# Kernel tuning notes

Hardware: AMD Instinct MI355X
Metric: run time of the kernel (lower is better)

Reference implementation:

```python
import jax, jax.numpy as jnp
import numpy as np

C = 0.01          # Poincare ball curvature 1/100
SQRT_C = 0.1
EPS = 1e-15
BALL_EPS = 4e-3   # geoopt float32 projx boundary epsilon


def _norm(x):
    return jnp.linalg.norm(x, axis=-1, keepdims=True)


def expmap0(u):
    n = jnp.maximum(_norm(u), EPS)
    return jnp.tanh(SQRT_C * n) * u / (SQRT_C * n)


def logmap0(x):
    n = jnp.maximum(_norm(x), EPS)
    t = jnp.clip(SQRT_C * n, -1.0 + 1e-7, 1.0 - 1e-7)
    return jnp.arctanh(t) * x / (SQRT_C * n)


def projx(x):
    maxnorm = (1.0 - BALL_EPS) / SQRT_C
    n = jnp.maximum(_norm(x), EPS)
    return jnp.where(n > maxnorm, x / n * maxnorm, x)


def mobius_matvec(M, x):
    xn = jnp.maximum(_norm(x), EPS)
    mx = x @ M.T
    mxn = jnp.maximum(_norm(mx), EPS)
    t = jnp.clip(SQRT_C * xn, -1.0 + 1e-7, 1.0 - 1e-7)
    res = jnp.tanh(mxn / xn * jnp.arctanh(t)) * mx / (mxn * SQRT_C)
    return jnp.where(jnp.all(mx == 0, axis=-1, keepdims=True), 0.0, res)


def mobius_add(x, y):
    x2 = jnp.sum(x * x, -1, keepdims=True)
    y2 = jnp.sum(y * y, -1, keepdims=True)
    xy = jnp.sum(x * y, -1, keepdims=True)
    num = (1 + 2 * C * xy + C * y2) * x + (1 - C * x2) * y
    den = 1 + 2 * C * xy + C * C * x2 * y2
    return num / jnp.maximum(den, EPS)


def hyp_linear(x, W, b):
    # eval mode: weight dropout is a no-op
    res = projx(mobius_matvec(W, x))
    hb = projx(expmap0(b.reshape(1, -1)))
    return projx(mobius_add(res, hb))


def setup_inputs() -> dict:
    key = jax.random.key(0)
    ks = jax.random.split(key, 10)
    B, S, N, H, HEADS, E = 2, 4, 10000, 64, 4, 160000
    G = B * S
    OC = H // HEADS
    # edges guaranteed to have no self-loops (module removes then re-adds them)
    src = jax.random.randint(ks[0], (G, E), 0, N)
    off = jax.random.randint(ks[1], (G, E), 1, N)
    dst = (src + off) % N
    edge_index = jnp.stack([src, dst], axis=1).astype(jnp.int32)  # [G,2,E]

    def glorot(k, shape, fan):
        a = np.sqrt(6.0 / fan)
        return jax.random.uniform(k, shape, minval=-a, maxval=a, dtype=jnp.float32)

    emb = jax.random.normal(ks[2], (N, H), dtype=jnp.float32)
    att_i = glorot(ks[3], (1, HEADS, OC), HEADS * OC + 1)
    att_j = glorot(ks[4], (1, HEADS, OC), HEADS * OC + 1)
    w1 = glorot(ks[5], (H, OC), H + OC)   # HypLinear(in=16, out=64): weight [out,in]
    b1 = jnp.zeros((H,), jnp.float32)
    w2 = glorot(ks[6], (H, H), H + H)
    b2 = jnp.zeros((H,), jnp.float32)
    history_graphs = jnp.zeros((B, S, N), jnp.float32)  # only shape is used
    return {"history_graphs": history_graphs, "edge_index": edge_index,
            "emb": emb, "att_i": att_i, "att_j": att_j,
            "w1": w1, "b1": b1, "w2": w2, "b2": b2}


def reference(history_graphs, edge_index, emb, att_i, att_j, w1, b1, w2, b2):
    B, S, N = history_graphs.shape
    G = edge_index.shape[0]
    H = emb.shape[1]
    heads = att_i.shape[1]
    oc = H // heads

    # node ids are arange(N) for every (b,s) -> identical features per graph
    x0 = projx(expmap0(emb))   # initHyperX, [N,H]
    xt = logmap0(x0)           # tangent features used by attention, [N,H]

    # add self loops (inputs contain none)
    loops = jnp.broadcast_to(jnp.arange(N, dtype=edge_index.dtype)[None, None, :], (G, 2, N))
    ei = jnp.concatenate([edge_index, loops], axis=-1)  # [G,2,E+N]

    def agg(e):
        src, dst = e[0], e[1]                       # targets (i), sources (j)
        x_i = xt[src].reshape(-1, heads, oc)        # [E2,h,oc]
        x_j = xt[dst].reshape(-1, heads, oc)
        alpha = jnp.sum(x_i * att_i, -1) + jnp.sum(x_j * att_j, -1)  # [E2,h]
        alpha = jax.nn.leaky_relu(alpha, 0.2)
        m = jax.ops.segment_max(alpha, src, num_segments=N)
        a = jnp.exp(alpha - m[src])
        s = jax.ops.segment_sum(a, src, num_segments=N)
        a = a / (s[src] + 1e-16)                    # edge softmax; dropout eval no-op
        sup = jax.ops.segment_sum(x_j * a[..., None], src, num_segments=N)  # [N,h,oc]
        sup = sup.mean(axis=1)                      # concat=False -> head mean, [N,oc]
        return projx(expmap0(sup))

    h = jax.vmap(agg)(ei)                           # [G,N,oc]
    node_emb = h.reshape(B, S, N, oc)[:, -1]        # last timestep, [B,N,oc]

    z = hyp_linear(node_emb, w1, b1)                # 16 -> 64
    z = projx(expmap0(jax.nn.silu(logmap0(z))))     # HypAct(SiLU)
    z = projx(expmap0(logmap0(z)))                  # HypDropout (eval: log/exp round trip)
    z = hyp_linear(z, w2, b2)                       # 64 -> 64
    return z
```

## Files before the change

### kernel.cpp

```cpp
#include <hip/hip_runtime.h>
#include <hip/hip_bf16.h>

#define N_NODES 10000
#define NE 160000
#define CAP 96
#define SQRT_C 0.1f
#define CC 0.01f
#define EPS 1e-15f
#define MAXNORM ((1.0f - 4e-3f) / SQRT_C)

__device__ __forceinline__ float ldf(const void* p, int i, int isbf) {
    return isbf ? __bfloat162float(((const __hip_bfloat16*)p)[i])
                : ((const float*)p)[i];
}

__device__ __forceinline__ float wsum(float v) {
#pragma unroll
    for (int off = 32; off > 0; off >>= 1) v += __shfl_xor(v, off, 64);
    return v;
}
__device__ __forceinline__ float wmax(float v) {
#pragma unroll
    for (int off = 32; off > 0; off >>= 1) v = fmaxf(v, __shfl_xor(v, off, 64));
    return v;
}

__global__ __launch_bounds__(256) void init_sniff(int* __restrict__ cnt,
                                                  int* __restrict__ ovf_cnt,
                                                  const unsigned* __restrict__ embw,
                                                  int* __restrict__ flag) {
    int t = blockIdx.x * 256 + threadIdx.x;
    if (t < 2 * N_NODES) cnt[t] = 0;
    if (t == 0) *ovf_cnt = 0;
    if (blockIdx.x == 0 && threadIdx.x < 64) {
        unsigned w = embw[threadIdx.x];
        unsigned e = (w >> 7) & 0xFFu;
        unsigned long long m = __ballot(e >= 116u && e <= 133u);
        if (threadIdx.x == 0) *flag = (__popcll(m) >= 32) ? 1 : 0;
    }
}

#define EDGE_PREAMBLE(T)                                                  \
    int slot = ((T) >= NE) ? 1 : 0;                                       \
    int e = (T) - slot * NE;                                              \
    int g = slot ? 7 : 3;

__global__ __launch_bounds__(256) void pre_scatter(const void* __restrict__ emb,
                                                   const void* __restrict__ att_i,
                                                   const void* __restrict__ att_j,
                                                   const void* __restrict__ w1g,
                                                   const void* __restrict__ b1g,
                                                   const void* __restrict__ w2g,
                                                   const void* __restrict__ b2g,
                                                   const int* __restrict__ flag,
                                                   const int* __restrict__ ei,
                                                   float* __restrict__ xt,
                                                   float* __restrict__ ai,
                                                   float* __restrict__ aj,
                                                   int* __restrict__ cnt,
                                                   unsigned short* __restrict__ bucket,
                                                   int* __restrict__ ovf_cnt,
                                                   unsigned* __restrict__ ovf,
                                                   float* __restrict__ wf1t,
                                                   float* __restrict__ wf2t,
                                                   float* __restrict__ hb1f,
                                                   float* __restrict__ hb2f,
                                                   float* __restrict__ hbn2) {
    if (blockIdx.x < 2500) {
        int isbf = *flag;
        int t = blockIdx.x * 256 + threadIdx.x;
        int node = t >> 6;
        int lane = t & 63;
        float u = ldf(emb, node * 64 + lane, isbf);
        float n = fmaxf(sqrtf(wsum(u * u)), EPS);
        float th = tanhf(SQRT_C * n);
        float x0 = th / (SQRT_C * n) * u;
        float x0n = th / SQRT_C;
        if (x0n > MAXNORM) { x0 *= MAXNORM / x0n; x0n = MAXNORM; }
        float tc = fminf(SQRT_C * x0n, 1.0f - 1e-7f);
        float xv = atanhf(tc) / (SQRT_C * x0n) * x0;
        xt[node * 64 + lane] = xv;
        float pi = xv * ldf(att_i, lane, isbf);
        float pj = xv * ldf(att_j, lane, isbf);
#pragma unroll
        for (int off = 8; off > 0; off >>= 1) {
            pi += __shfl_xor(pi, off, 64);
            pj += __shfl_xor(pj, off, 64);
        }
        if ((lane & 15) == 0) {
            ai[node * 4 + (lane >> 4)] = pi;
            aj[node * 4 + (lane >> 4)] = pj;
        }
    } else if (blockIdx.x < 3750) {
        int t = (blockIdx.x - 2500) * 256 + threadIdx.x;
        EDGE_PREAMBLE(t);
        int src = ei[g * 2 * NE + e];
        int dst = ei[g * 2 * NE + NE + e];
        int i = slot * N_NODES + src;
        int pos = atomicAdd(&cnt[i], 1);
        if (pos < CAP) bucket[i * CAP + pos] = (unsigned short)dst;
        else {
            int oi = atomicAdd(ovf_cnt, 1);
            ovf[oi] = ((unsigned)slot << 28) | ((unsigned)src << 14) | (unsigned)dst;
        }
    } else {
        int isbf = *flag;
        int tid = threadIdx.x;
        for (int i = tid; i < 1024; i += 256) {
            int o = i >> 4, c = i & 15;
            wf1t[c * 64 + o] = ldf(w1g, i, isbf);
        }
        for (int i = tid; i < 4096; i += 256) {
            int o = i >> 6, c = i & 63;
            wf2t[c * 64 + o] = ldf(w2g, i, isbf);
        }
        int w = tid >> 6, lane = tid & 63;
        if (w < 2) {
            const void* bg = w ? b2g : b1g;
            float b = ldf(bg, lane, isbf);
            float n = fmaxf(sqrtf(wsum(b * b)), EPS);
            float th = tanhf(SQRT_C * n);
            float hv = th / (SQRT_C * n) * b;
            float hn = th / SQRT_C;
            if (hn > MAXNORM) { hv *= MAXNORM / hn; hn = MAXNORM; }
            (w ? hb2f : hb1f)[lane] = hv;
            if (lane == 0) hbn2[w] = hn * hn;
        }
    }
}

__global__ __launch_bounds__(256) void node_agg(const int* __restrict__ cnt,
                                                const unsigned short* __restrict__ bucket,
                                                const int* __restrict__ ovf_cnt,
                                                const unsigned* __restrict__ ovf,
                                                const float* __restrict__ ai,
                                                const float* __restrict__ aj,
                                                const float* __restrict__ xt,
                                                float* __restrict__ sup_t) {
    __shared__ float wlds[4][64 * 4];
    __shared__ int dlds[4][64];
    int w = threadIdx.x >> 6, lane = threadIdx.x & 63;
    int idx = blockIdx.x * 4 + w;
    int slot = (idx >= N_NODES) ? 1 : 0;
    int n = idx - slot * N_NODES;
    int deg = cnt[idx];
    int start = idx * CAP;

    float4 ai4 = *(const float4*)&ai[n * 4];
    float4 aj4n = *(const float4*)&aj[n * 4];
    float ain[4] = {ai4.x, ai4.y, ai4.z, ai4.w};
    float ajn[4] = {aj4n.x, aj4n.y, aj4n.z, aj4n.w};
    int hh = lane >> 4;
    float acc;

    if (deg <= 63) {
        bool act = (lane <= deg);
        int d = (lane < deg) ? (int)bucket[start + lane] : n;
        float4 a4 = act ? *(const float4*)&aj[d * 4] : make_float4(0.f, 0.f, 0.f, 0.f);
        float ajv[4] = {a4.x, a4.y, a4.z, a4.w};
        float al[4], mh[4], eh[4];
#pragma unroll
        for (int h = 0; h < 4; ++h) {
            float a = ain[h] + ajv[h];
            a = (a < 0.0f) ? 0.2f * a : a;
            al[h] = act ? a : -1e30f;
            mh[h] = al[h];
        }
#pragma unroll
        for (int h = 0; h < 4; ++h) mh[h] = wmax(mh[h]);
#pragma unroll
        for (int h = 0; h < 4; ++h) eh[h] = act ? expf(al[h] - mh[h]) : 0.0f;
        float sh[4];
#pragma unroll
        for (int h = 0; h < 4; ++h) sh[h] = wsum(eh[h]);
#pragma unroll
        for (int h = 0; h < 4; ++h)
            wlds[w][lane * 4 + h] = eh[h] * (0.25f / (sh[h] + 1e-16f));
        dlds[w][lane] = d;
        int m = deg + 1;
        float a0 = 0.f, a1 = 0.f, a2 = 0.f, a3 = 0.f;
        int e = 0;
        for (; e + 4 <= m; e += 4) {
            int d0 = dlds[w][e], d1 = dlds[w][e + 1];
            int d2 = dlds[w][e + 2], d3 = dlds[w][e + 3];
            float w0 = wlds[w][(e + 0) * 4 + hh], w1 = wlds[w][(e + 1) * 4 + hh];
            float w2 = wlds[w][(e + 2) * 4 + hh], w3 = wlds[w][(e + 3) * 4 + hh];
            a0 = fmaf(w0, xt[d0 * 64 + lane], a0);
            a1 = fmaf(w1, xt[d1 * 64 + lane], a1);
            a2 = fmaf(w2, xt[d2 * 64 + lane], a2);
            a3 = fmaf(w3, xt[d3 * 64 + lane], a3);
        }
        for (; e < m; ++e)
            a0 = fmaf(wlds[w][e * 4 + hh], xt[dlds[w][e] * 64 + lane], a0);
        acc = (a0 + a1) + (a2 + a3);
    } else {
        int bdeg = (deg < CAP) ? deg : CAP;
        int tov = (deg > CAP) ? *ovf_cnt : 0;
        float mh[4];
#pragma unroll
        for (int h = 0; h < 4; ++h) {
            float a = ain[h] + ajn[h];
            mh[h] = (a < 0.0f) ? 0.2f * a : a;
        }
        for (int e = lane; e < bdeg; e += 64) {
            int d = bucket[start + e];
#pragma unroll
            for (int h = 0; h < 4; ++h) {
                float a = ain[h] + aj[d * 4 + h];
                a = (a < 0.0f) ? 0.2f * a : a;
                mh[h] = fmaxf(mh[h], a);
            }
        }
        for (int k = lane; k < tov; k += 64) {
            unsigned pe = ovf[k];
            if ((int)(pe >> 28) == slot && (int)((pe >> 14) & 0x3FFFu) == n) {
                int d = pe & 0x3FFFu;
#pragma unroll
                for (int h = 0; h < 4; ++h) {
                    float a = ain[h] + aj[d * 4 + h];
                    a = (a < 0.0f) ? 0.2f * a : a;
                    mh[h] = fmaxf(mh[h], a);
                }
            }
        }
#pragma unroll
        for (int h = 0; h < 4; ++h) mh[h] = wmax(mh[h]);
        float sh[4] = {0.f, 0.f, 0.f, 0.f};
        if (lane == 0) {
#pragma unroll
            for (int h = 0; h < 4; ++h) {
                float a = ain[h] + ajn[h];
                a = (a < 0.0f) ? 0.2f * a : a;
                sh[h] = expf(a - mh[h]);
            }
        }
        for (int e = lane; e < bdeg; e += 64) {
            int d = bucket[start + e];
#pragma unroll
            for (int h = 0; h < 4; ++h) {
                float a = ain[h] + aj[d * 4 + h];
                a = (a < 0.0f) ? 0.2f * a : a;
                sh[h] += expf(a - mh[h]);
            }
        }
        for (int k = lane; k < tov; k += 64) {
            unsigned pe = ovf[k];
            if ((int)(pe >> 28) == slot && (int)((pe >> 14) & 0x3FFFu) == n) {
                int d = pe & 0x3FFFu;
#pragma unroll
                for (int h = 0; h < 4; ++h) {
                    float a = ain[h] + aj[d * 4 + h];
                    a = (a < 0.0f) ? 0.2f * a : a;
                    sh[h] += expf(a - mh[h]);
                }
            }
        }
#pragma unroll
        for (int h = 0; h < 4; ++h) sh[h] = wsum(sh[h]);
        float scale[4];
#pragma unroll
        for (int h = 0; h < 4; ++h) scale[h] = 0.25f / (sh[h] + 1e-16f);
        float aih = ain[hh], mhh = mh[hh], sch = scale[hh];
        float aself = aih + ajn[hh];
        aself = (aself < 0.0f) ? 0.2f * aself : aself;
        acc = expf(aself - mhh) * sch * xt[n * 64 + lane];
        for (int e = 0; e < bdeg; ++e) {
            int d = bucket[start + e];
            float a = aih + aj[d * 4 + hh];
            a = (a < 0.0f) ? 0.2f * a : a;
            acc = fmaf(expf(a - mhh) * sch, xt[d * 64 + lane], acc);
        }
        for (int k = 0; k < tov; ++k) {
            unsigned pe = ovf[k];
            if ((int)(pe >> 28) == slot && (int)((pe >> 14) & 0x3FFFu) == n) {
                int d = pe & 0x3FFFu;
                float a = aih + aj[d * 4 + hh];
                a = (a < 0.0f) ? 0.2f * a : a;
                acc = fmaf(expf(a - mhh) * sch, xt[d * 64 + lane], acc);
            }
        }
    }
    acc += __shfl_xor(acc, 16, 64);
    acc += __shfl_xor(acc, 32, 64);
    if (lane < 16) sup_t[lane * 20000 + idx] = acc;
}

__global__ __launch_bounds__(256) void final_stage(const float* __restrict__ sup_t,
                                                   const float* __restrict__ wf1t,
                                                   const float* __restrict__ wf2t,
                                                   const float* __restrict__ hb1f,
                                                   const float* __restrict__ hb2f,
                                                   const float* __restrict__ hbn2,
                                                   const int* __restrict__ flag,
                                                   void* __restrict__ outv) {
    __shared__ float Z[65 * 64];
    __shared__ float pA[2][4][64];
    __shared__ float pB[2][4][64];
    int w = threadIdx.x >> 6, lane = threadIdx.x & 63;
    int base = blockIdx.x * 64;
    int nd = base + lane;
    bool valid = (nd < 2 * N_NODES);
    int isbf = *flag;
    float y2a = hbn2[0], y2b = hbn2[1];
    int ob = w * 16;

    float v[16];
#pragma unroll
    for (int c = 0; c < 16; ++c) v[c] = valid ? sup_t[c * 20000 + nd] : 0.0f;
    float n2 = 0.f;
#pragma unroll
    for (int c = 0; c < 16; ++c) n2 = fmaf(v[c], v[c], n2);
    float n = fmaxf(sqrtf(n2), EPS);
    float th0 = tanhf(SQRT_C * n);
    float s0 = th0 / (SQRT_C * n);
    float x0n = th0 / SQRT_C;
    if (x0n > MAXNORM) { s0 *= MAXNORM / x0n; x0n = MAXNORM; }
#pragma unroll
    for (int c = 0; c < 16; ++c) v[c] *= s0;

    float a1[16];
#pragma unroll
    for (int oj = 0; oj < 16; ++oj) a1[oj] = 0.f;
#pragma unroll
    for (int c = 0; c < 16; ++c) {
        float vc = v[c];
#pragma unroll
        for (int oj = 0; oj < 16; ++oj)
            a1[oj] = fmaf(wf1t[c * 64 + ob + oj], vc, a1[oj]);
    }
    float pn = 0.f, ph = 0.f;
#pragma unroll
    for (int oj = 0; oj < 16; ++oj) {
        pn = fmaf(a1[oj], a1[oj], pn);
        ph = fmaf(a1[oj], hb1f[ob + oj], ph);
    }
    pA[0][w][lane] = pn; pA[1][w][lane] = ph;
    __syncthreads();
    float mxn2 = pA[0][0][lane] + pA[0][1][lane] + pA[0][2][lane] + pA[0][3][lane];
    float mxhb = pA[1][0][lane] + pA[1][1][lane] + pA[1][2][lane] + pA[1][3][lane];

    float z2n;
    {
        float xn = fmaxf(x0n, EPS);
        float mxn = fmaxf(sqrtf(mxn2), EPS);
        float t = fminf(SQRT_C * xn, 1.0f - 1e-7f);
        float th = tanhf(mxn / xn * atanhf(t));
        float rs = th / (mxn * SQRT_C);
        float rn = th / SQRT_C;
        if (mxn2 == 0.0f) { rs = 0.f; rn = 0.f; }
        if (rn > MAXNORM) { rs *= MAXNORM / rn; rn = MAXNORM; }
        float xy = rs * mxhb;
        float x2 = rn * rn;
        float A = 1.0f + 2.0f * CC * xy + CC * y2a;
        float B = 1.0f - CC * x2;
        float rden = 1.0f / fmaxf(1.0f + 2.0f * CC * xy + CC * CC * x2 * y2a, EPS);
        float pz = 0.f;
#pragma unroll
        for (int oj = 0; oj < 16; ++oj) {
            float z = (A * rs * a1[oj] + B * hb1f[ob + oj]) * rden;
            a1[oj] = z;
            pz = fmaf(z, z, pz);
        }
        pB[0][w][lane] = pz;
        __syncthreads();
        float zn2 = pB[0][0][lane] + pB[0][1][lane] + pB[0][2][lane] + pB[0][3][lane];
        float zn = fmaxf(sqrtf(zn2), EPS);
        float sc = (zn > MAXNORM) ? MAXNORM / zn : 1.0f;
        float z1n = fminf(zn, MAXNORM);
        float lg = atanhf(fminf(SQRT_C * z1n, 1.0f - 1e-7f)) / (SQRT_C * z1n) * sc;
        float pu = 0.f;
#pragma unroll
        for (int oj = 0; oj < 16; ++oj) {
            float u = lg * a1[oj];
            u = u / (1.0f + expf(-u));
            a1[oj] = u;
            pu = fmaf(u, u, pu);
        }
        pA[0][w][lane] = pu;
        __syncthreads();
        float un2 = pA[0][0][lane] + pA[0][1][lane] + pA[0][2][lane] + pA[0][3][lane];
        float un = fmaxf(sqrtf(un2), EPS);
        float th2 = tanhf(SQRT_C * un);
        float s2 = th2 / (SQRT_C * un);
        z2n = th2 / SQRT_C;
        if (z2n > MAXNORM) { s2 *= MAXNORM / z2n; z2n = MAXNORM; }
#pragma unroll
        for (int oj = 0; oj < 16; ++oj) Z[(ob + oj) * 64 + lane] = a1[oj] * s2;
    }
    __syncthreads();

    float a2[16];
#pragma unroll
    for (int oj = 0; oj < 16; ++oj) a2[oj] = 0.f;
#pragma unroll 4
    for (int c = 0; c < 64; ++c) {
        float zc = Z[c * 64 + lane];
#pragma unroll
        for (int oj = 0; oj < 16; ++oj)
            a2[oj] = fmaf(wf2t[c * 64 + ob + oj], zc, a2[oj]);
    }
    float pn2 = 0.f, ph2 = 0.f;
#pragma unroll
    for (int oj = 0; oj < 16; ++oj) {
        pn2 = fmaf(a2[oj], a2[oj], pn2);
        ph2 = fmaf(a2[oj], hb2f[ob + oj], ph2);
    }
    pB[0][w][lane] = pn2; pB[1][w][lane] = ph2;
    __syncthreads();
    float mxn2b = pB[0][0][lane] + pB[0][1][lane] + pB[0][2][lane] + pB[0][3][lane];
    float mxhb2 = pB[1][0][lane] + pB[1][1][lane] + pB[1][2][lane] + pB[1][3][lane];
    {
        float xn = fmaxf(z2n, EPS);
        float mxn = fmaxf(sqrtf(mxn2b), EPS);
        float t = fminf(SQRT_C * xn, 1.0f - 1e-7f);
        float th = tanhf(mxn / xn * atanhf(t));
        float rs = th / (mxn * SQRT_C);
        float rn = th / SQRT_C;
        if (mxn2b == 0.0f) { rs = 0.f; rn = 0.f; }
        if (rn > MAXNORM) { rs *= MAXNORM / rn; rn = MAXNORM; }
        float xy = rs * mxhb2;
        float x2 = rn * rn;
        float A = 1.0f + 2.0f * CC * xy + CC * y2b;
        float B = 1.0f - CC * x2;
        float rden = 1.0f / fmaxf(1.0f + 2.0f * CC * xy + CC * CC * x2 * y2b, EPS);
        float pz = 0.f;
#pragma unroll
        for (int oj = 0; oj < 16; ++oj) {
            float z = (A * rs * a2[oj] + B * hb2f[ob + oj]) * rden;
            a2[oj] = z;
            pz = fmaf(z, z, pz);
        }
        pA[0][w][lane] = pz;
        __syncthreads();
        float zn2 = pA[0][0][lane] + pA[0][1][lane] + pA[0][2][lane] + pA[0][3][lane];
        float zn = fmaxf(sqrtf(zn2), EPS);
        float s4 = (zn > MAXNORM) ? MAXNORM / zn : 1.0f;
#pragma unroll
        for (int oj = 0; oj < 16; ++oj) Z[(ob + oj) * 65 + lane] = a2[oj] * s4;
    }
    __syncthreads();

#pragma unroll 1
    for (int k = 0; k < 16; ++k) {
        int nl = w * 16 + k;
        int ng = base + nl;
        if (ng >= 2 * N_NODES) break;
        float val = Z[lane * 65 + nl];
        if (isbf) ((__hip_bfloat16*)outv)[ng * 64 + lane] = __float2bfloat16(val);
        else      ((float*)outv)[ng * 64 + lane] = val;
    }
}

extern "C" void kernel_launch(void* const* d_in, const int* in_sizes, int n_in,
                              void* d_out, int out_size, void* d_ws, size_t ws_size,
                              hipStream_t stream) {
    const int* ei = (const int*)d_in[1];
    const void* emb   = d_in[2];
    const void* att_i = d_in[3];
    const void* att_j = d_in[4];
    const void* w1 = d_in[5];
    const void* b1 = d_in[6];
    const void* w2 = d_in[7];
    const void* b2 = d_in[8];

    float* ws = (float*)d_ws;
    float* xt    = ws;
    float* ai    = ws + 640000;
    float* aj    = ws + 680000;
    float* sup_t = ws + 720000;
    int* cnt   = (int*)(ws + 1040000);
    unsigned short* bucket = (unsigned short*)(ws + 1060000);
    unsigned* ovf = (unsigned*)(ws + 2020000);
    int* ovf_cnt  = (int*)(ws + 2340000);
    int* flag     = (int*)(ws + 2340001);
    float* wf1t = ws + 2340032;
    float* wf2t = ws + 2341056;
    float* hb1f = ws + 2345152;
    float* hb2f = ws + 2345216;
    float* hbn2 = ws + 2345280;

    hipLaunchKernelGGL(init_sniff, dim3(79), dim3(256), 0, stream,
                       cnt, ovf_cnt, (const unsigned*)emb, flag);
    hipLaunchKernelGGL(pre_scatter, dim3(3751), dim3(256), 0, stream,
                       emb, att_i, att_j, w1, b1, w2, b2, flag, ei,
                       xt, ai, aj, cnt, bucket, ovf_cnt, ovf,
                       wf1t, wf2t, hb1f, hb2f, hbn2);
    hipLaunchKernelGGL(node_agg, dim3(5000), dim3(256), 0, stream,
                       cnt, bucket, ovf_cnt, ovf, ai, aj, xt, sup_t);
    hipLaunchKernelGGL(final_stage, dim3(313), dim3(256), 0, stream,
                       sup_t, wf1t, wf2t, hb1f, hb2f, hbn2, flag, d_out);
}
```

Before: 155.4 us.

## Fuse four kernel launches into one persistent kernel with grid barriers

Replaces the four separate launches (init, pre-scatter, node aggregation, final stage) with a single persistent kernel of 768 blocks that loops over the original block indices. Stages are separated by custom global atomic barriers that use open and done sentinel values. The goal is to remove the launch gaps and tail effects between small kernels. In exchange it relies on all 768 blocks being co-resident, adds spin-wait barrier latency, and grid-strides the work, which may lower per-stage parallelism.

Result: slower. 606.4 us (+290.3%).

```diff
diff --git a/kernel.cpp b/kernel.cpp
--- a/kernel.cpp
+++ b/kernel.cpp
@@ -4,6 +4,7 @@
 #define N_NODES 10000
 #define NE 160000
 #define CAP 96
+#define GRID 768
 #define SQRT_C 0.1f
 #define CC 0.01f
 #define EPS 1e-15f
@@ -25,19 +26,30 @@
     return v;
 }
 
-__global__ __launch_bounds__(256) void init_sniff(int* __restrict__ cnt,
-                                                  int* __restrict__ ovf_cnt,
-                                                  const unsigned* __restrict__ embw,
-                                                  int* __restrict__ flag) {
-    int t = blockIdx.x * 256 + threadIdx.x;
-    if (t < 2 * N_NODES) cnt[t] = 0;
-    if (t == 0) *ovf_cnt = 0;
-    if (blockIdx.x == 0 && threadIdx.x < 64) {
-        unsigned w = embw[threadIdx.x];
-        unsigned e = (w >> 7) & 0xFFu;
-        unsigned long long m = __ballot(e >= 116u && e <= 133u);
-        if (threadIdx.x == 0) *flag = (__popcll(m) >= 32) ? 1 : 0;
+#define M_OPEN(i) (0x13570000 + 2 * (i))
+#define M_DONE(i) (0x13570001 + 2 * (i))
+__device__ __forceinline__ void gbar(int* cnt, int* gen, int i, int G) {
+    __syncthreads();
+    if (threadIdx.x == 0) {
+        __threadfence();
+        for (long k = 0; k < (1L << 26); ++k) {
+            if (__hip_atomic_load(gen, __ATOMIC_ACQUIRE, __HIP_MEMORY_SCOPE_AGENT)
+                == M_OPEN(i)) break;
+            __builtin_amdgcn_s_sleep(8);
+        }
+        if (atomicAdd(cnt, 1) == G - 1) {
+            __hip_atomic_store(gen, M_DONE(i), __ATOMIC_RELEASE,
+                               __HIP_MEMORY_SCOPE_AGENT);
+        } else {
+            for (long k = 0; k < (1L << 26); ++k) {
+                if (__hip_atomic_load(gen, __ATOMIC_ACQUIRE, __HIP_MEMORY_SCOPE_AGENT)
+                    == M_DONE(i)) break;
+                __builtin_amdgcn_s_sleep(8);
+            }
+        }
     }
+    __syncthreads();
+    __threadfence();
 }
 
 #define EDGE_PREAMBLE(T)                                                  \
@@ -45,176 +57,185 @@
     int e = (T) - slot * NE;                                              \
     int g = slot ? 7 : 3;
 
-__global__ __launch_bounds__(256) void pre_scatter(const void* __restrict__ emb,
-                                                   const void* __restrict__ att_i,
-                                                   const void* __restrict__ att_j,
-                                                   const void* __restrict__ w1g,
-                                                   const void* __restrict__ b1g,
-                                                   const void* __restrict__ w2g,
-                                                   const void* __restrict__ b2g,
-                                                   const int* __restrict__ flag,
-                                                   const int* __restrict__ ei,
-                                                   float* __restrict__ xt,
-                                                   float* __restrict__ ai,
-                                                   float* __restrict__ aj,
-                                                   int* __restrict__ cnt,
-                                                   unsigned short* __restrict__ bucket,
-                                                   int* __restrict__ ovf_cnt,
-                                                   unsigned* __restrict__ ovf,
-                                                   float* __restrict__ wf1t,
-                                                   float* __restrict__ wf2t,
-                                                   float* __restrict__ hb1f,
-                                                   float* __restrict__ hb2f,
-                                                   float* __restrict__ hbn2) {
-    if (blockIdx.x < 2500) {
-        int isbf = *flag;
-        int t = blockIdx.x * 256 + threadIdx.x;
-        int node = t >> 6;
-        int lane = t & 63;
-        float u = ldf(emb, node * 64 + lane, isbf);
-        float n = fmaxf(sqrtf(wsum(u * u)), EPS);
-        float th = tanhf(SQRT_C * n);
-        float x0 = th / (SQRT_C * n) * u;
-        float x0n = th / SQRT_C;
-        if (x0n > MAXNORM) { x0 *= MAXNORM / x0n; x0n = MAXNORM; }
-        float tc = fminf(SQRT_C * x0n, 1.0f - 1e-7f);
-        float xv = atanhf(tc) / (SQRT_C * x0n) * x0;
-        xt[node * 64 + lane] = xv;
-        float pi = xv * ldf(att_i, lane, isbf);
-        float pj = xv * ldf(att_j, lane, isbf);
-#pragma unroll
-        for (int off = 8; off > 0; off >>= 1) {
-            pi += __shfl_xor(pi, off, 64);
-            pj += __shfl_xor(pj, off, 64);
-        }
-        if ((lane & 15) == 0) {
-            ai[node * 4 + (lane >> 4)] = pi;
-            aj[node * 4 + (lane >> 4)] = pj;
-        }
-    } else if (blockIdx.x < 3750) {
-        int t = (blockIdx.x - 2500) * 256 + threadIdx.x;
-        EDGE_PREAMBLE(t);
-        int src = ei[g * 2 * NE + e];
-        int dst = ei[g * 2 * NE + NE + e];
-        int i = slot * N_NODES + src;
-        int pos = atomicAdd(&cnt[i], 1);
-        if (pos < CAP) bucket[i * CAP + pos] = (unsigned short)dst;
-        else {
-            int oi = atomicAdd(ovf_cnt, 1);
-            ovf[oi] = ((unsigned)slot << 28) | ((unsigned)src << 14) | (unsigned)dst;
-        }
-    } else {
-        int isbf = *flag;
-        int tid = threadIdx.x;
-        for (int i = tid; i < 1024; i += 256) {
-            int o = i >> 4, c = i & 15;
-            wf1t[c * 64 + o] = ldf(w1g, i, isbf);
-        }
-        for (int i = tid; i < 4096; i += 256) {
-            int o = i >> 6, c = i & 63;
-            wf2t[c * 64 + o] = ldf(w2g, i, isbf);
-        }
-        int w = tid >> 6, lane = tid & 63;
-        if (w < 2) {
-            const void* bg = w ? b2g : b1g;
-            float b = ldf(bg, lane, isbf);
-            float n = fmaxf(sqrtf(wsum(b * b)), EPS);
+__global__ __launch_bounds__(256, 4) void fused(const int* __restrict__ ei,
+                                                const void* __restrict__ emb,
+                                                const void* __restrict__ att_i,
+                                                const void* __restrict__ att_j,
+                                                const void* __restrict__ w1g,
+                                                const void* __restrict__ b1g,
+                                                const void* __restrict__ w2g,
+                                                const void* __restrict__ b2g,
+                                                float* __restrict__ xt,
+                                                float* __restrict__ ai,
+                                                float* __restrict__ aj,
+                                                float* __restrict__ sup_t,
+                                                int* __restrict__ cnt,
+                                                unsigned short* __restrict__ bucket,
+                                                int* __restrict__ ovf_cnt,
+                                                unsigned* __restrict__ ovf,
+                                                int* __restrict__ flag,
+                                                float* __restrict__ wf1t,
+                                                float* __restrict__ wf2t,
+                                                float* __restrict__ hb1f,
+                                                float* __restrict__ hb2f,
+                                                float* __restrict__ hbn2,
+                                                int* __restrict__ bar,
+                                                void* __restrict__ outv) {
+    __shared__ float smem[5184];
+    const int G = gridDim.x;
+    int tid = threadIdx.x;
+    int w = tid >> 6, lane = tid & 63;
+
+    for (int t = blockIdx.x * 256 + tid; t < 2 * N_NODES; t += G * 256) cnt[t] = 0;
+    if (blockIdx.x == 0 && tid < 64) {
+        unsigned wv = ((const unsigned*)emb)[tid];
+        unsigned ex = (wv >> 7) & 0xFFu;
+        unsigned long long m = __ballot(ex >= 116u && ex <= 133u);
+        if (tid == 0) {
+            *flag = (__popcll(m) >= 32) ? 1 : 0;
+            *ovf_cnt = 0;
+            bar[0] = 0; bar[32] = 0; bar[64] = 0;
+            __threadfence();
+            __hip_atomic_store(&bar[16], M_OPEN(0), __ATOMIC_RELEASE,
+                               __HIP_MEMORY_SCOPE_AGENT);
+            __hip_atomic_store(&bar[48], M_OPEN(1), __ATOMIC_RELEASE,
+                               __HIP_MEMORY_SCOPE_AGENT);
+            __hip_atomic_store(&bar[80], M_OPEN(2), __ATOMIC_RELEASE,
+                               __HIP_MEMORY_SCOPE_AGENT);
+        }
+    }
+    gbar(&bar[0], &bar[16], 0, G);
+    int isbf = *flag;
+
+    for (int lb = blockIdx.x; lb < 3751; lb += G) {
+        if (lb < 2500) {
+            int t = lb * 256 + tid;
+            int node = t >> 6;
+            float u = ldf(emb, node * 64 + lane, isbf);
+            float n = fmaxf(sqrtf(wsum(u * u)), EPS);
             float th = tanhf(SQRT_C * n);
-            float hv = th / (SQRT_C * n) * b;
-            float hn = th / SQRT_C;
-            if (hn > MAXNORM) { hv *= MAXNORM / hn; hn = MAXNORM; }
-            (w ? hb2f : hb1f)[lane] = hv;
-            if (lane == 0) hbn2[w] = hn * hn;
+            float x0 = th / (SQRT_C * n) * u;
+            float x0n = th / SQRT_C;
+            if (x0n > MAXNORM) { x0 *= MAXNORM / x0n; x0n = MAXNORM; }
+            float tc = fminf(SQRT_C * x0n, 1.0f - 1e-7f);
+            float xv = atanhf(tc) / (SQRT_C * x0n) * x0;
+            xt[node * 64 + lane] = xv;
+            float pi = xv * ldf(att_i, lane, isbf);
+            float pj = xv * ldf(att_j, lane, isbf);
+#pragma unroll
+            for (int off = 8; off > 0; off >>= 1) {
+                pi += __shfl_xor(pi, off, 64);
+                pj += __shfl_xor(pj, off, 64);
+            }
+            if ((lane & 15) == 0) {
+                ai[node * 4 + (lane >> 4)] = pi;
+                aj[node * 4 + (lane >> 4)] = pj;
+            }
+        } else if (lb < 3750) {
+            int t = (lb - 2500) * 256 + tid;
+            EDGE_PREAMBLE(t);
+            int src = ei[g * 2 * NE + e];
+            int dst = ei[g * 2 * NE + NE + e];
+            int i = slot * N_NODES + src;
+            int pos = atomicAdd(&cnt[i], 1);
+            if (pos < CAP) bucket[i * CAP + pos] = (unsigned short)dst;
+            else {
+                int oi = atomicAdd(ovf_cnt, 1);
+                ovf[oi] = ((unsigned)slot << 28) | ((unsigned)src << 14) | (unsigned)dst;
+            }
+        } else {
+            for (int i = tid; i < 1024; i += 256) {
+                int o = i >> 4, c = i & 15;
+                wf1t[c * 64 + o] = ldf(w1g, i, isbf);
+            }
+            for (int i = tid; i < 4096; i += 256) {
+                int o = i >> 6, c = i & 63;
+                wf2t[c * 64 + o] = ldf(w2g, i, isbf);
+            }
+            if (w < 2) {
+                const void* bg = w ? b2g : b1g;
+                float b = ldf(bg, lane, isbf);
+                float n = fmaxf(sqrtf(wsum(b * b)), EPS);
+                float th = tanhf(SQRT_C * n);
+                float hv = th / (SQRT_C * n) * b;
+                float hn = th / SQRT_C;
+                if (hn > MAXNORM) { hv *= MAXNORM / hn; hn = MAXNORM; }
+                (w ? hb2f : hb1f)[lane] = hv;
+                if (lane == 0) hbn2[w] = hn * hn;
+            }
         }
     }
-}
-
-__global__ __launch_bounds__(256) void node_agg(const int* __restrict__ cnt,
-                                                const unsigned short* __restrict__ bucket,
-                                                const int* __restrict__ ovf_cnt,
-                                                const unsigned* __restrict__ ovf,
-                                                const float* __restrict__ ai,
-                                                const float* __restrict__ aj,
-                                                const float* __restrict__ xt,
-                                                float* __restrict__ sup_t) {
-    __shared__ float wlds[4][64 * 4];
-    __shared__ int dlds[4][64];
-    int w = threadIdx.x >> 6, lane = threadIdx.x & 63;
-    int idx = blockIdx.x * 4 + w;
-    int slot = (idx >= N_NODES) ? 1 : 0;
-    int n = idx - slot * N_NODES;
-    int deg = cnt[idx];
-    int start = idx * CAP;
-
-    float4 ai4 = *(const float4*)&ai[n * 4];
-    float4 aj4n = *(const float4*)&aj[n * 4];
-    float ain[4] = {ai4.x, ai4.y, ai4.z, ai4.w};
-    float ajn[4] = {aj4n.x, aj4n.y, aj4n.z, aj4n.w};
-    int hh = lane >> 4;
-    float acc;
-
-    if (deg <= 63) {
-        bool act = (lane <= deg);
-        int d = (lane < deg) ? (int)bucket[start + lane] : n;
-        float4 a4 = act ? *(const float4*)&aj[d * 4] : make_float4(0.f, 0.f, 0.f, 0.f);
-        float ajv[4] = {a4.x, a4.y, a4.z, a4.w};
-        float al[4], mh[4], eh[4];
-#pragma unroll
-        for (int h = 0; h < 4; ++h) {
-            float a = ain[h] + ajv[h];
-            a = (a < 0.0f) ? 0.2f * a : a;
-            al[h] = act ? a : -1e30f;
-            mh[h] = al[h];
-        }
-#pragma unroll
-        for (int h = 0; h < 4; ++h) mh[h] = wmax(mh[h]);
-#pragma unroll
-        for (int h = 0; h < 4; ++h) eh[h] = act ? expf(al[h] - mh[h]) : 0.0f;
-        float sh[4];
-#pragma unroll
-        for (int h = 0; h < 4; ++h) sh[h] = wsum(eh[h]);
-#pragma unroll
-        for (int h = 0; h < 4; ++h)
-            wlds[w][lane * 4 + h] = eh[h] * (0.25f / (sh[h] + 1e-16f));
-        dlds[w][lane] = d;
-        int m = deg + 1;
-        float a0 = 0.f, a1 = 0.f, a2 = 0.f, a3 = 0.f;
-        int e = 0;
-        for (; e + 4 <= m; e += 4) {
-            int d0 = dlds[w][e], d1 = dlds[w][e + 1];
-            int d2 = dlds[w][e + 2], d3 = dlds[w][e + 3];
-            float w0 = wlds[w][(e + 0) * 4 + hh], w1 = wlds[w][(e + 1) * 4 + hh];
-            float w2 = wlds[w][(e + 2) * 4 + hh], w3 = wlds[w][(e + 3) * 4 + hh];
-            a0 = fmaf(w0, xt[d0 * 64 + lane], a0);
-            a1 = fmaf(w1, xt[d1 * 64 + lane], a1);
-            a2 = fmaf(w2, xt[d2 * 64 + lane], a2);
-            a3 = fmaf(w3, xt[d3 * 64 + lane], a3);
-        }
-        for (; e < m; ++e)
-            a0 = fmaf(wlds[w][e * 4 + hh], xt[dlds[w][e] * 64 + lane], a0);
-        acc = (a0 + a1) + (a2 + a3);
-    } else {
-        int bdeg = (deg < CAP) ? deg : CAP;
-        int tov = (deg > CAP) ? *ovf_cnt : 0;
-        float mh[4];
-#pragma unroll
-        for (int h = 0; h < 4; ++h) {
-            float a = ain[h] + ajn[h];
-            mh[h] = (a < 0.0f) ? 0.2f * a : a;
-        }
-        for (int e = lane; e < bdeg; e += 64) {
-            int d = bucket[start + e];
+    gbar(&bar[32], &bar[48], 1, G);
+
+    float* wlds = smem;
+    int* dlds = (int*)&smem[1024];
+    for (int lb = blockIdx.x; lb < 5000; lb += G) {
+        int idx = lb * 4 + w;
+        int slot = (idx >= N_NODES) ? 1 : 0;
+        int n = idx - slot * N_NODES;
+        int deg = cnt[idx];
+        int start = idx * CAP;
+
+        float4 ai4 = *(const float4*)&ai[n * 4];
+        float4 aj4n = *(const float4*)&aj[n * 4];
+        float ain[4] = {ai4.x, ai4.y, ai4.z, ai4.w};
+        float ajn[4] = {aj4n.x, aj4n.y, aj4n.z, aj4n.w};
+        int hh = lane >> 4;
+        float acc;
+
+        if (deg <= 63) {
+            bool act = (lane <= deg);
+            int d = (lane < deg) ? (int)bucket[start + lane] : n;
+            float4 a4 = act ? *(const float4*)&aj[d * 4] : make_float4(0.f, 0.f, 0.f, 0.f);
+            float ajv[4] = {a4.x, a4.y, a4.z, a4.w};
+            float al[4], mh[4], eh[4];
 #pragma unroll
             for (int h = 0; h < 4; ++h) {
-                float a = ain[h] + aj[d * 4 + h];
+                float a = ain[h] + ajv[h];
                 a = (a < 0.0f) ? 0.2f * a : a;
-                mh[h] = fmaxf(mh[h], a);
-            }
-        }
-        for (int k = lane; k < tov; k += 64) {
-            unsigned pe = ovf[k];
-            if ((int)(pe >> 28) == slot && (int)((pe >> 14) & 0x3FFFu) == n) {
-                int d = pe & 0x3FFFu;
+                al[h] = act ? a : -1e30f;
+                mh[h] = al[h];
+            }
+#pragma unroll
+            for (int h = 0; h < 4; ++h) mh[h] = wmax(mh[h]);
+#pragma unroll
+            for (int h = 0; h < 4; ++h) eh[h] = act ? expf(al[h] - mh[h]) : 0.0f;
+            float sh[4];
+#pragma unroll
+            for (int h = 0; h < 4; ++h) sh[h] = wsum(eh[h]);
+#pragma unroll
+            for (int h = 0; h < 4; ++h)
+                wlds[w * 256 + lane * 4 + h] = eh[h] * (0.25f / (sh[h] + 1e-16f));
+            dlds[w * 64 + lane] = d;
+            int m = deg + 1;
+            float a0 = 0.f, a1 = 0.f, a2 = 0.f, a3 = 0.f;
+            int e = 0;
+            for (; e + 4 <= m; e += 4) {
+                int d0 = dlds[w * 64 + e], d1 = dlds[w * 64 + e + 1];
+                int d2 = dlds[w * 64 + e + 2], d3 = dlds[w * 64 + e + 3];
+                float w0 = wlds[w * 256 + (e + 0) * 4 + hh];
+                float w1 = wlds[w * 256 + (e + 1) * 4 + hh];
+                float w2 = wlds[w * 256 + (e + 2) * 4 + hh];
+                float w3 = wlds[w * 256 + (e + 3) * 4 + hh];
+                a0 = fmaf(w0, xt[d0 * 64 + lane], a0);
+                a1 = fmaf(w1, xt[d1 * 64 + lane], a1);
+                a2 = fmaf(w2, xt[d2 * 64 + lane], a2);
+                a3 = fmaf(w3, xt[d3 * 64 + lane], a3);
+            }
+            for (; e < m; ++e)
+                a0 = fmaf(wlds[w * 256 + e * 4 + hh], xt[dlds[w * 64 + e] * 64 + lane], a0);
+            acc = (a0 + a1) + (a2 + a3);
+        } else {
+            int bdeg = (deg < CAP) ? deg : CAP;
+            int tov = (deg > CAP) ? *ovf_cnt : 0;
+            float mh[4];
+#pragma unroll
+            for (int h = 0; h < 4; ++h) {
+                float a = ain[h] + ajn[h];
+                mh[h] = (a < 0.0f) ? 0.2f * a : a;
+            }
+            for (int e = lane; e < bdeg; e += 64) {
+                int d = bucket[start + e];
 #pragma unroll
                 for (int h = 0; h < 4; ++h) {
                     float a = ain[h] + aj[d * 4 + h];
@@ -222,31 +243,31 @@
                     mh[h] = fmaxf(mh[h], a);
                 }
             }
-        }
-#pragma unroll
-        for (int h = 0; h < 4; ++h) mh[h] = wmax(mh[h]);
-        float sh[4] = {0.f, 0.f, 0.f, 0.f};
-        if (lane == 0) {
-#pragma unroll
-            for (int h = 0; h < 4; ++h) {
-                float a = ain[h] + ajn[h];
-                a = (a < 0.0f) ? 0.2f * a : a;
-                sh[h] = expf(a - mh[h]);
-            }
-        }
-        for (int e = lane; e < bdeg; e += 64) {
-            int d = bucket[start + e];
-#pragma unroll
-            for (int h = 0; h < 4; ++h) {
-                float a = ain[h] + aj[d * 4 + h];
-                a = (a < 0.0f) ? 0.2f * a : a;
-                sh[h] += expf(a - mh[h]);
-            }
-        }
-        for (int k = lane; k < tov; k += 64) {
-            unsigned pe = ovf[k];
-            if ((int)(pe >> 28) == slot && (int)((pe >> 14) & 0x3FFFu) == n) {
-                int d = pe & 0x3FFFu;
+            for (int k = lane; k < tov; k += 64) {
+                unsigned pe = ovf[k];
+                if ((int)(pe >> 28) == slot && (int)((pe >> 14) & 0x3FFFu) == n) {
+                    int d = pe & 0x3FFFu;
+#pragma unroll
+                    for (int h = 0; h < 4; ++h) {
+                        float a = ain[h] + aj[d * 4 + h];
+                        a = (a < 0.0f) ? 0.2f * a : a;
+                        mh[h] = fmaxf(mh[h], a);
+                    }
+                }
+            }
+#pragma unroll
+            for (int h = 0; h < 4; ++h) mh[h] = wmax(mh[h]);
+            float sh[4] = {0.f, 0.f, 0.f, 0.f};
+            if (lane == 0) {
+#pragma unroll
+                for (int h = 0; h < 4; ++h) {
+                    float a = ain[h] + ajn[h];
+                    a = (a < 0.0f) ? 0.2f * a : a;
+                    sh[h] = expf(a - mh[h]);
+                }
+            }
+            for (int e = lane; e < bdeg; e += 64) {
+                int d = bucket[start + e];
 #pragma unroll
                 for (int h = 0; h < 4; ++h) {
                     float a = ain[h] + aj[d * 4 + h];
@@ -254,200 +275,209 @@
                     sh[h] += expf(a - mh[h]);
                 }
             }
-        }
-#pragma unroll
-        for (int h = 0; h < 4; ++h) sh[h] = wsum(sh[h]);
-        float scale[4];
-#pragma unroll
-        for (int h = 0; h < 4; ++h) scale[h] = 0.25f / (sh[h] + 1e-16f);
-        float aih = ain[hh], mhh = mh[hh], sch = scale[hh];
-        float aself = aih + ajn[hh];
-        aself = (aself < 0.0f) ? 0.2f * aself : aself;
-        acc = expf(aself - mhh) * sch * xt[n * 64 + lane];
-        for (int e = 0; e < bdeg; ++e) {
-            int d = bucket[start + e];
-            float a = aih + aj[d * 4 + hh];
-            a = (a < 0.0f) ? 0.2f * a : a;
-            acc = fmaf(expf(a - mhh) * sch, xt[d * 64 + lane], acc);
-        }
-        for (int k = 0; k < tov; ++k) {
-            unsigned pe = ovf[k];
-            if ((int)(pe >> 28) == slot && (int)((pe >> 14) & 0x3FFFu) == n) {
-                int d = pe & 0x3FFFu;
+            for (int k = lane; k < tov; k += 64) {
+                unsigned pe = ovf[k];
+                if ((int)(pe >> 28) == slot && (int)((pe >> 14) & 0x3FFFu) == n) {
+                    int d = pe & 0x3FFFu;
+#pragma unroll
+                    for (int h = 0; h < 4; ++h) {
+                        float a = ain[h] + aj[d * 4 + h];
+                        a = (a < 0.0f) ? 0.2f * a : a;
+                        sh[h] += expf(a - mh[h]);
+                    }
+                }
+            }
+#pragma unroll
+            for (int h = 0; h < 4; ++h) sh[h] = wsum(sh[h]);
+            float scale[4];
+#pragma unroll
+            for (int h = 0; h < 4; ++h) scale[h] = 0.25f / (sh[h] + 1e-16f);
+            float aih = ain[hh], mhh = mh[hh], sch = scale[hh];
+            float aself = aih + ajn[hh];
+            aself = (aself < 0.0f) ? 0.2f * aself : aself;
+            acc = expf(aself - mhh) * sch * xt[n * 64 + lane];
+            for (int e = 0; e < bdeg; ++e) {
+                int d = bucket[start + e];
                 float a = aih + aj[d * 4 + hh];
                 a = (a < 0.0f) ? 0.2f * a : a;
                 acc = fmaf(expf(a - mhh) * sch, xt[d * 64 + lane], acc);
             }
-        }
+            for (int k = 0; k < tov; ++k) {
+                unsigned pe = ovf[k];
+                if ((int)(pe >> 28) == slot && (int)((pe >> 14) & 0x3FFFu) == n) {
+                    int d = pe & 0x3FFFu;
+                    float a = aih + aj[d * 4 + hh];
+                    a = (a < 0.0f) ? 0.2f * a : a;
+                    acc = fmaf(expf(a - mhh) * sch, xt[d * 64 + lane], acc);
+                }
+            }
+        }
+        acc += __shfl_xor(acc, 16, 64);
+        acc += __shfl_xor(acc, 32, 64);
+        if (lane < 16) sup_t[lane * 20000 + idx] = acc;
     }
-    acc += __shfl_xor(acc, 16, 64);
-    acc += __shfl_xor(acc, 32, 64);
-    if (lane < 16) sup_t[lane * 20000 + idx] = acc;
-}
-
-__global__ __launch_bounds__(256) void final_stage(const float* __restrict__ sup_t,
-                                                   const float* __restrict__ wf1t,
-                                                   const float* __restrict__ wf2t,
-                                                   const float* __restrict__ hb1f,
-                                                   const float* __restrict__ hb2f,
-                                                   const float* __restrict__ hbn2,
-                                                   const int* __restrict__ flag,
-                                                   void* __restrict__ outv) {
-    __shared__ float Z[65 * 64];
-    __shared__ float pA[2][4][64];
-    __shared__ float pB[2][4][64];
-    int w = threadIdx.x >> 6, lane = threadIdx.x & 63;
-    int base = blockIdx.x * 64;
-    int nd = base + lane;
-    bool valid = (nd < 2 * N_NODES);
-    int isbf = *flag;
-    float y2a = hbn2[0], y2b = hbn2[1];
-    int ob = w * 16;
-
-    float v[16];
-#pragma unroll
-    for (int c = 0; c < 16; ++c) v[c] = valid ? sup_t[c * 20000 + nd] : 0.0f;
-    float n2 = 0.f;
-#pragma unroll
-    for (int c = 0; c < 16; ++c) n2 = fmaf(v[c], v[c], n2);
-    float n = fmaxf(sqrtf(n2), EPS);
-    float th0 = tanhf(SQRT_C * n);
-    float s0 = th0 / (SQRT_C * n);
-    float x0n = th0 / SQRT_C;
-    if (x0n > MAXNORM) { s0 *= MAXNORM / x0n; x0n = MAXNORM; }
-#pragma unroll
-    for (int c = 0; c < 16; ++c) v[c] *= s0;
-
-    float a1[16];
-#pragma unroll
-    for (int oj = 0; oj < 16; ++oj) a1[oj] = 0.f;
-#pragma unroll
-    for (int c = 0; c < 16; ++c) {
-        float vc = v[c];
-#pragma unroll
-        for (int oj = 0; oj < 16; ++oj)
-            a1[oj] = fmaf(wf1t[c * 64 + ob + oj], vc, a1[oj]);
-    }
-    float pn = 0.f, ph = 0.f;
-#pragma unroll
-    for (int oj = 0; oj < 16; ++oj) {
-        pn = fmaf(a1[oj], a1[oj], pn);
-        ph = fmaf(a1[oj], hb1f[ob + oj], ph);
-    }
-    pA[0][w][lane] = pn; pA[1][w][lane] = ph;
-    __syncthreads();
-    float mxn2 = pA[0][0][lane] + pA[0][1][lane] + pA[0][2][lane] + pA[0][3][lane];
-    float mxhb = pA[1][0][lane] + pA[1][1][lane] + pA[1][2][lane] + pA[1][3][lane];
-
-    float z2n;
-    {
-        float xn = fmaxf(x0n, EPS);
-        float mxn = fmaxf(sqrtf(mxn2), EPS);
-        float t = fminf(SQRT_C * xn, 1.0f - 1e-7f);
-        float th = tanhf(mxn / xn * atanhf(t));
-        float rs = th / (mxn * SQRT_C);
-        float rn = th / SQRT_C;
-        if (mxn2 == 0.0f) { rs = 0.f; rn = 0.f; }
-        if (rn > MAXNORM) { rs *= MAXNORM / rn; rn = MAXNORM; }
-        float xy = rs * mxhb;
-        float x2 = rn * rn;
-        float A = 1.0f + 2.0f * CC * xy + CC * y2a;
-        float B = 1.0f - CC * x2;
-        float rden = 1.0f / fmaxf(1.0f + 2.0f * CC * xy + CC * CC * x2 * y2a, EPS);
-        float pz = 0.f;
+    gbar(&bar[64], &bar[80], 2, G);
+
+    float* Z = smem;
+    float* pA = &smem[4160];
+    float* pB = &smem[4672];
+    for (int lb = blockIdx.x; lb < 313; lb += G) {
+        int base = lb * 64;
+        int nd = base + lane;
+        bool valid = (nd < 2 * N_NODES);
+        float y2a = hbn2[0], y2b = hbn2[1];
+        int ob = w * 16;
+
+        float v[16];
+#pragma unroll
+        for (int c = 0; c < 16; ++c) v[c] = valid ? sup_t[c * 20000 + nd] : 0.0f;
+        float n2 = 0.f;
+#pragma unroll
+        for (int c = 0; c < 16; ++c) n2 = fmaf(v[c], v[c], n2);
+        float n = fmaxf(sqrtf(n2), EPS);
+        float th0 = tanhf(SQRT_C * n);
+        float s0 = th0 / (SQRT_C * n);
+        float x0n = th0 / SQRT_C;
+        if (x0n > MAXNORM) { s0 *= MAXNORM / x0n; x0n = MAXNORM; }
+#pragma unroll
+        for (int c = 0; c < 16; ++c) v[c] *= s0;
+
+        float a1[16];
+#pragma unroll
+        for (int oj = 0; oj < 16; ++oj) a1[oj] = 0.f;
+#pragma unroll
+        for (int c = 0; c < 16; ++c) {
+            float vc = v[c];
+#pragma unroll
+            for (int oj = 0; oj < 16; ++oj)
+                a1[oj] = fmaf(wf1t[c * 64 + ob + oj], vc, a1[oj]);
+        }
+        float pn = 0.f, ph = 0.f;
 #pragma unroll
         for (int oj = 0; oj < 16; ++oj) {
-            float z = (A * rs * a1[oj] + B * hb1f[ob + oj]) * rden;
-            a1[oj] = z;
-            pz = fmaf(z, z, pz);
-        }
-        pB[0][w][lane] = pz;
+            pn = fmaf(a1[oj], a1[oj], pn);
+            ph = fmaf(a1[oj], hb1f[ob + oj], ph);
+        }
+        pA[0 * 256 + w * 64 + lane] = pn; pA[1 * 256 + w * 64 + lane] = ph;
         __syncthreads();
-        float zn2 = pB[0][0][lane] + pB[0][1][lane] + pB[0][2][lane] + pB[0][3][lane];
-        float zn = fmaxf(sqrtf(zn2), EPS);
-        float sc = (zn > MAXNORM) ? MAXNORM / zn : 1.0f;
-        float z1n = fminf(zn, MAXNORM);
-        float lg = atanhf(fminf(SQRT_C * z1n, 1.0f - 1e-7f)) / (SQRT_C * z1n) * sc;
-        float pu = 0.f;
+        float mxn2 = pA[0 * 256 + lane] + pA[0 * 256 + 64 + lane] +
+                     pA[0 * 256 + 128 + lane] + pA[0 * 256 + 192 + lane];
+        float mxhb = pA[1 * 256 + lane] + pA[1 * 256 + 64 + lane] +
+                     pA[1 * 256 + 128 + lane] + pA[1 * 256 + 192 + lane];
+
+        float z2n;
+        {
+            float xn = fmaxf(x0n, EPS);
+            float mxn = fmaxf(sqrtf(mxn2), EPS);
+            float t = fminf(SQRT_C * xn, 1.0f - 1e-7f);
+            float th = tanhf(mxn / xn * atanhf(t));
+            float rs = th / (mxn * SQRT_C);
+            float rn = th / SQRT_C;
+            if (mxn2 == 0.0f) { rs = 0.f; rn = 0.f; }
+            if (rn > MAXNORM) { rs *= MAXNORM / rn; rn = MAXNORM; }
+            float xy = rs * mxhb;
+            float x2 = rn * rn;
+            float A = 1.0f + 2.0f * CC * xy + CC * y2a;
+            float B = 1.0f - CC * x2;
+            float rden = 1.0f / fmaxf(1.0f + 2.0f * CC * xy + CC * CC * x2 * y2a, EPS);
+            float pz = 0.f;
+#pragma unroll
+            for (int oj = 0; oj < 16; ++oj) {
+                float z = (A * rs * a1[oj] + B * hb1f[ob + oj]) * rden;
+                a1[oj] = z;
+                pz = fmaf(z, z, pz);
+            }
+            pB[w * 64 + lane] = pz;
+            __syncthreads();
+            float zn2 = pB[lane] + pB[64 + lane] + pB[128 + lane] + pB[192 + lane];
+            float zn = fmaxf(sqrtf(zn2), EPS);
+            float sc = (zn > MAXNORM) ? MAXNORM / zn : 1.0f;
+            float z1n = fminf(zn, MAXNORM);
+            float lg = atanhf(fminf(SQRT_C * z1n, 1.0f - 1e-7f)) / (SQRT_C * z1n) * sc;
+            float pu = 0.f;
+#pragma unroll
+            for (int oj = 0; oj < 16; ++oj) {
+                float u = lg * a1[oj];
+                u = u / (1.0f + expf(-u));
+                a1[oj] = u;
+                pu = fmaf(u, u, pu);
+            }
+            pA[w * 64 + lane] = pu;
+            __syncthreads();
+            float un2 = pA[lane] + pA[64 + lane] + pA[128 + lane] + pA[192 + lane];
+            float un = fmaxf(sqrtf(un2), EPS);
+            float th2 = tanhf(SQRT_C * un);
+            float s2 = th2 / (SQRT_C * un);
+            z2n = th2 / SQRT_C;
+            if (z2n > MAXNORM) { s2 *= MAXNORM / z2n; z2n = MAXNORM; }
+#pragma unroll
+            for (int oj = 0; oj < 16; ++oj) Z[(ob + oj) * 64 + lane] = a1[oj] * s2;
+        }
+        __syncthreads();
+
+        float a2[16];
+#pragma unroll
+        for (int oj = 0; oj < 16; ++oj) a2[oj] = 0.f;
+#pragma unroll 4
+        for (int c = 0; c < 64; ++c) {
+            float zc = Z[c * 64 + lane];
+#pragma unroll
+            for (int oj = 0; oj < 16; ++oj)
+                a2[oj] = fmaf(wf2t[c * 64 + ob + oj], zc, a2[oj]);
+        }
+        float pn2 = 0.f, ph2 = 0.f;
 #pragma unroll
         for (int oj = 0; oj < 16; ++oj) {
-            float u = lg * a1[oj];
-            u = u / (1.0f + expf(-u));
-            a1[oj] = u;
-            pu = fmaf(u, u, pu);
-        }
-        pA[0][w][lane] = pu;
+            pn2 = fmaf(a2[oj], a2[oj], pn2);
+            ph2 = fmaf(a2[oj], hb2f[ob + oj], ph2);
+        }
+        pB[0 * 256 + w * 64 + lane] = pn2; pB[1 * 256 + w * 64 + lane] = ph2;
         __syncthreads();
-        float un2 = pA[0][0][lane] + pA[0][1][lane] + pA[0][2][lane] + pA[0][3][lane];
-        float un = fmaxf(sqrtf(un2), EPS);
-        float th2 = tanhf(SQRT_C * un);
-        float s2 = th2 / (SQRT_C * un);
-        z2n = th2 / SQRT_C;
-        if (z2n > MAXNORM) { s2 *= MAXNORM / z2n; z2n = MAXNORM; }
-#pragma unroll
-        for (int oj = 0; oj < 16; ++oj) Z[(ob + oj) * 64 + lane] = a1[oj] * s2;
-    }
-    __syncthreads();
-
-    float a2[16];
-#pragma unroll
-    for (int oj = 0; oj < 16; ++oj) a2[oj] = 0.f;
-#pragma unroll 4
-    for (int c = 0; c < 64; ++c) {
-        float zc = Z[c * 64 + lane];
-#pragma unroll
-        for (int oj = 0; oj < 16; ++oj)
-            a2[oj] = fmaf(wf2t[c * 64 + ob + oj], zc, a2[oj]);
-    }
-    float pn2 = 0.f, ph2 = 0.f;
-#pragma unroll
-    for (int oj = 0; oj < 16; ++oj) {
-        pn2 = fmaf(a2[oj], a2[oj], pn2);
-        ph2 = fmaf(a2[oj], hb2f[ob + oj], ph2);
-    }
-    pB[0][w][lane] = pn2; pB[1][w][lane] = ph2;
-    __syncthreads();
-    float mxn2b = pB[0][0][lane] + pB[0][1][lane] + pB[0][2][lane] + pB[0][3][lane];
-    float mxhb2 = pB[1][0][lane] + pB[1][1][lane] + pB[1][2][lane] + pB[1][3][lane];
-    {
-        float xn = fmaxf(z2n, EPS);
-        float mxn = fmaxf(sqrtf(mxn2b), EPS);
-        float t = fminf(SQRT_C * xn, 1.0f - 1e-7f);
-        float th = tanhf(mxn / xn * atanhf(t));
-        float rs = th / (mxn * SQRT_C);
-        float rn = th / SQRT_C;
-        if (mxn2b == 0.0f) { rs = 0.f; rn = 0.f; }
-        if (rn > MAXNORM) { rs *= MAXNORM / rn; rn = MAXNORM; }
-        float xy = rs * mxhb2;
-        float x2 = rn * rn;
-        float A = 1.0f + 2.0f * CC * xy + CC * y2b;
-        float B = 1.0f - CC * x2;
-        float rden = 1.0f / fmaxf(1.0f + 2.0f * CC * xy + CC * CC * x2 * y2b, EPS);
-        float pz = 0.f;
-#pragma unroll
-        for (int oj = 0; oj < 16; ++oj) {
-            float z = (A * rs * a2[oj] + B * hb2f[ob + oj]) * rden;
-            a2[oj] = z;
-            pz = fmaf(z, z, pz);
-        }
-        pA[0][w][lane] = pz;
+        float mxn2b = pB[0 * 256 + lane] + pB[0 * 256 + 64 + lane] +
+                      pB[0 * 256 + 128 + lane] + pB[0 * 256 + 192 + lane];
+        float mxhb2 = pB[1 * 256 + lane] + pB[1 * 256 + 64 + lane] +
+                      pB[1 * 256 + 128 + lane] + pB[1 * 256 + 192 + lane];
+        {
+            float xn = fmaxf(z2n, EPS);
+            float mxn = fmaxf(sqrtf(mxn2b), EPS);
+            float t = fminf(SQRT_C * xn, 1.0f - 1e-7f);
+            float th = tanhf(mxn / xn * atanhf(t));
+            float rs = th / (mxn * SQRT_C);
+            float rn = th / SQRT_C;
+            if (mxn2b == 0.0f) { rs = 0.f; rn = 0.f; }
+            if (rn > MAXNORM) { rs *= MAXNORM / rn; rn = MAXNORM; }
+            float xy = rs * mxhb2;
+            float x2 = rn * rn;
+            float A = 1.0f + 2.0f * CC * xy + CC * y2b;
+            float B = 1.0f - CC * x2;
+            float rden = 1.0f / fmaxf(1.0f + 2.0f * CC * xy + CC * CC * x2 * y2b, EPS);
+            float pz = 0.f;
+#pragma unroll
+            for (int oj = 0; oj < 16; ++oj) {
+                float z = (A * rs * a2[oj] + B * hb2f[ob + oj]) * rden;
+                a2[oj] = z;
+                pz = fmaf(z, z, pz);
+            }
+            pA[w * 64 + lane] = pz;
+            __syncthreads();
+            float zn2 = pA[lane] + pA[64 + lane] + pA[128 + lane] + pA[192 + lane];
+            float zn = fmaxf(sqrtf(zn2), EPS);
+            float s4 = (zn > MAXNORM) ? MAXNORM / zn : 1.0f;
+#pragma unroll
+            for (int oj = 0; oj < 16; ++oj) Z[(ob + oj) * 65 + lane] = a2[oj] * s4;
+        }
         __syncthreads();
-        float zn2 = pA[0][0][lane] + pA[0][1][lane] + pA[0][2][lane] + pA[0][3][lane];
-        float zn = fmaxf(sqrtf(zn2), EPS);
-        float s4 = (zn > MAXNORM) ? MAXNORM / zn : 1.0f;
-#pragma unroll
-        for (int oj = 0; oj < 16; ++oj) Z[(ob + oj) * 65 + lane] = a2[oj] * s4;
-    }
-    __syncthreads();
 
 #pragma unroll 1
-    for (int k = 0; k < 16; ++k) {
-        int nl = w * 16 + k;
-        int ng = base + nl;
-        if (ng >= 2 * N_NODES) break;
-        float val = Z[lane * 65 + nl];
-        if (isbf) ((__hip_bfloat16*)outv)[ng * 64 + lane] = __float2bfloat16(val);
-        else      ((float*)outv)[ng * 64 + lane] = val;
+        for (int k = 0; k < 16; ++k) {
+            int nl = w * 16 + k;
+            int ng = base + nl;
+            if (ng >= 2 * N_NODES) break;
+            float val = Z[lane * 65 + nl];
+            if (isbf) ((__hip_bfloat16*)outv)[ng * 64 + lane] = __float2bfloat16(val);
+            else      ((float*)outv)[ng * 64 + lane] = val;
+        }
+        __syncthreads();
     }
 }
 
@@ -478,15 +508,10 @@
     float* hb1f = ws + 2345152;
     float* hb2f = ws + 2345216;
     float* hbn2 = ws + 2345280;
-
-    hipLaunchKernelGGL(init_sniff, dim3(79), dim3(256), 0, stream,
-                       cnt, ovf_cnt, (const unsigned*)emb, flag);
-    hipLaunchKernelGGL(pre_scatter, dim3(3751), dim3(256), 0, stream,
-                       emb, att_i, att_j, w1, b1, w2, b2, flag, ei,
-                       xt, ai, aj, cnt, bucket, ovf_cnt, ovf,
-                       wf1t, wf2t, hb1f, hb2f, hbn2);
-    hipLaunchKernelGGL(node_agg, dim3(5000), dim3(256), 0, stream,
-                       cnt, bucket, ovf_cnt, ovf, ai, aj, xt, sup_t);
-    hipLaunchKernelGGL(final_stage, dim3(313), dim3(256), 0, stream,
-                       sup_t, wf1t, wf2t, hb1f, hb2f, hbn2, flag, d_out);
+    int* bar    = (int*)(ws + 2345344);
+
+    hipLaunchKernelGGL(fused, dim3(GRID), dim3(256), 0, stream,
+                       ei, emb, att_i, att_j, w1, b1, w2, b2,
+                       xt, ai, aj, sup_t, cnt, bucket, ovf_cnt, ovf,
+                       flag, wf1t, wf2t, hb1f, hb2f, hbn2, bar, d_out);
 }
```
